# Optimization experiments

Measured on AMD Instinct MI355X. Metric: run time of the kernel, lower is better.

## Reference

```python
import jax, jax.numpy as jnp
import numpy as np

B, H, L, E = 32, 8, 512, 3
N_VARS = 8
TOP_P = 0.5
NOISE_EPS = 0.01
EPS = 1e-10


def setup_inputs() -> dict:
    key = jax.random.key(0)
    k1, k2, k3 = jax.random.split(key, 3)
    scale = 1.0 / np.sqrt(L)  # sane logits for softmax
    x = jax.random.normal(k1, (B, H, L, L), dtype=jnp.float32)
    gate_w = jax.random.normal(k2, (E, L), dtype=jnp.float32) * scale
    noise_w = jax.random.normal(k3, (E, L), dtype=jnp.float32) * scale
    return {"x": x, "gate_w": gate_w, "noise_w": noise_w}


def _build_masks(L, n_vars):
    # Vectorized version of the torch per-k loop building [L, 3, L] masks.
    N = L // n_vars
    j = jnp.arange(L)          # target position
    k = jnp.arange(L)[:, None]  # source position
    S = ((j % N == k % N) & (j != k)).astype(jnp.float32)   # same offset, different var
    T = ((j // N) == (k // N)).astype(jnp.float32)           # same variable block
    ST = 1.0 - S - T
    return jnp.stack([S, T, ST], axis=1)  # [L, 3, L]


def _noisy_top_p_gating(xf, gate_w, noise_w, key):
    # xf: [BH, L, L] -> logits [BH, L, E]
    clean_logits = jnp.einsum('ble,ne->bln', xf, gate_w)
    noise_stddev = jax.nn.softplus(jnp.einsum('ble,ne->bln', xf, noise_w)) + NOISE_EPS
    noisy_logits = clean_logits + jax.random.normal(key, clean_logits.shape, clean_logits.dtype) * noise_stddev
    probs = jax.nn.softmax(noisy_logits, axis=-1)  # softmax over experts (dim 2)
    # dynamic (entropy) loss: sum over L dim (dim=1), mean over rest
    loss_dynamic = -(probs * jnp.log(probs + EPS)).sum(axis=1).mean()
    # sort descending over experts
    order = jnp.argsort(-probs, axis=-1)
    sorted_probs = jnp.take_along_axis(probs, order, axis=-1)
    cum = jnp.cumsum(sorted_probs, axis=-1)
    mask = cum > TOP_P
    # keep the first expert that crosses the threshold
    thr_idx = jnp.argmax(mask.astype(jnp.int32), axis=-1)          # [BH, L]
    thr_mask = jnp.arange(E) == thr_idx[..., None]                 # one-hot bool
    mask = mask & ~thr_mask
    # scatter kept (mask==0) sorted positions back to original expert ids:
    # top_p_mask[..., sorted_indices[..., k]] = (mask[..., k] == 0)
    inv = jnp.argsort(order, axis=-1)
    top_p_mask = jnp.take_along_axis((~mask).astype(jnp.float32), inv, axis=-1)
    # importance loss on masked sorted probs summed over batch dim
    kept = jnp.where(mask, 0.0, sorted_probs)
    importance = kept.sum(axis=0)  # [L, E]
    loss_importance = jnp.var(importance, ddof=1) / (importance.mean() ** 2 + EPS)
    loss = loss_importance + 0.1 * loss_dynamic
    return top_p_mask, loss


def reference(x, gate_w, noise_w):
    Bx, Hx, Lx, _ = x.shape
    xf = x.reshape(Bx * Hx, Lx, Lx)
    gates, loss = _noisy_top_p_gating(xf, gate_w, noise_w, jax.random.key(42))
    gates = gates.reshape(Bx, Hx, Lx, E).astype(jnp.float32)
    masks = _build_masks(Lx, N_VARS)            # [L, 3, L]
    mask_base = jnp.eye(Lx, dtype=jnp.float32)[None, None]
    out = jnp.einsum('bhli,lid->bhld', gates, masks) + mask_base
    return (out, loss)
```

## Files before the change

kernel.cpp:

```cpp
#include <hip/hip_runtime.h>
#include <cstdint>
#include <cstddef>


namespace {

constexpr int kBH = 256;
constexpr int kL = 512;
constexpr int kE = 3;
constexpr int kRows = kBH * kL;
constexpr int kPad = 36;

typedef float v4f __attribute__((ext_vector_type(4)));

__device__ __forceinline__ uint32_t rotl32(uint32_t v, int n) {
  return (v << n) | (v >> (32 - n));
}

__device__ __forceinline__ void threefry2x32_k42(uint32_t& x0, uint32_t& x1) {
  const uint32_t ks0 = 0u;
  const uint32_t ks1 = 42u;
  const uint32_t ks2 = 0u ^ 42u ^ 0x1BD11BDAu;
  x0 += ks0; x1 += ks1;
#define TF_ROUND(r) { x0 += x1; x1 = rotl32(x1, (r)); x1 ^= x0; }
  TF_ROUND(13) TF_ROUND(15) TF_ROUND(26) TF_ROUND(6)
  x0 += ks1; x1 += ks2 + 1u;
  TF_ROUND(17) TF_ROUND(29) TF_ROUND(16) TF_ROUND(24)
  x0 += ks2; x1 += ks0 + 2u;
  TF_ROUND(13) TF_ROUND(15) TF_ROUND(26) TF_ROUND(6)
  x0 += ks0; x1 += ks1 + 3u;
  TF_ROUND(17) TF_ROUND(29) TF_ROUND(16) TF_ROUND(24)
  x0 += ks1; x1 += ks2 + 4u;
  TF_ROUND(13) TF_ROUND(15) TF_ROUND(26) TF_ROUND(6)
  x0 += ks2; x1 += ks0 + 5u;
#undef TF_ROUND
}

__device__ __forceinline__ uint32_t jax_random_bits(uint32_t flat_idx) {
  uint32_t x0 = 0u;
  uint32_t x1 = flat_idx;
  threefry2x32_k42(x0, x1);
  return x0 ^ x1;
}

__device__ float bits_to_normal(uint32_t bits) {
#pragma clang fp contract(off)
  const uint32_t fb = (bits >> 9) | 0x3F800000u;
  const float f = __uint_as_float(fb) - 1.0f;
  const float lo = -0.99999994f;
  float u = f * 2.0f + lo;
  u = fmaxf(lo, u);
  float w = -log1pf(-(u * u));
  float p;
  if (w < 5.0f) {
    w = w - 2.5f;
    p = 2.81022636e-08f;
    p = 3.43273939e-07f + p * w;
    p = -3.5233877e-06f + p * w;
    p = -4.39150654e-06f + p * w;
    p = 0.00021858087f + p * w;
    p = -0.00125372503f + p * w;
    p = -0.00417768164f + p * w;
    p = 0.246640727f + p * w;
    p = 1.50140941f + p * w;
  } else {
    w = sqrtf(w) - 3.0f;
    p = -0.000200214257f;
    p = 0.000100950558f + p * w;
    p = 0.00134934322f + p * w;
    p = -0.00367342844f + p * w;
    p = 0.00573950773f + p * w;
    p = -0.0076224613f + p * w;
    p = 0.00943887047f + p * w;
    p = 1.00167406f + p * w;
    p = 2.83297682f + p * w;
  }
  const float einv = p * u;
  return 1.41421354f * einv;
}

__device__ __forceinline__ float softplus_f32(float v) {
#pragma clang fp contract(off)
  const float amax = fmaxf(v, 0.0f);
  return amax + log1pf(expf(-fabsf(v)));
}

#define COMP16(BUF, KB)                                                     \
  {                                                                         \
    _Pragma("unroll")                                                       \
    for (int j_ = 0; j_ < 4; ++j_) {                                        \
      const int k_ = (KB) + j_ * 4;                                         \
      const float4 wg0 = *reinterpret_cast<const float4*>(gw + k_);         \
      const float4 wg1 = *reinterpret_cast<const float4*>(gw + kL + k_);    \
      const float4 wg2 = *reinterpret_cast<const float4*>(gw + 2*kL + k_);  \
      const float4 wn0 = *reinterpret_cast<const float4*>(nw + k_);         \
      const float4 wn1 = *reinterpret_cast<const float4*>(nw + kL + k_);    \
      const float4 wn2 = *reinterpret_cast<const float4*>(nw + 2*kL + k_);  \
      const float4 xq = BUF[j_];                                            \
      accg[0] = fmaf(xq.x, wg0.x, accg[0]);                                 \
      accg[1] = fmaf(xq.x, wg1.x, accg[1]);                                 \
      accg[2] = fmaf(xq.x, wg2.x, accg[2]);                                 \
      accn[0] = fmaf(xq.x, wn0.x, accn[0]);                                 \
      accn[1] = fmaf(xq.x, wn1.x, accn[1]);                                 \
      accn[2] = fmaf(xq.x, wn2.x, accn[2]);                                 \
      accg[0] = fmaf(xq.y, wg0.y, accg[0]);                                 \
      accg[1] = fmaf(xq.y, wg1.y, accg[1]);                                 \
      accg[2] = fmaf(xq.y, wg2.y, accg[2]);                                 \
      accn[0] = fmaf(xq.y, wn0.y, accn[0]);                                 \
      accn[1] = fmaf(xq.y, wn1.y, accn[1]);                                 \
      accn[2] = fmaf(xq.y, wn2.y, accn[2]);                                 \
      accg[0] = fmaf(xq.z, wg0.z, accg[0]);                                 \
      accg[1] = fmaf(xq.z, wg1.z, accg[1]);                                 \
      accg[2] = fmaf(xq.z, wg2.z, accg[2]);                                 \
      accn[0] = fmaf(xq.z, wn0.z, accn[0]);                                 \
      accn[1] = fmaf(xq.z, wn1.z, accn[1]);                                 \
      accn[2] = fmaf(xq.z, wn2.z, accn[2]);                                 \
      accg[0] = fmaf(xq.w, wg0.w, accg[0]);                                 \
      accg[1] = fmaf(xq.w, wg1.w, accg[1]);                                 \
      accg[2] = fmaf(xq.w, wg2.w, accg[2]);                                 \
      accn[0] = fmaf(xq.w, wn0.w, accn[0]);                                 \
      accn[1] = fmaf(xq.w, wn1.w, accn[1]);                                 \
      accn[2] = fmaf(xq.w, wn2.w, accn[2]);                                 \
    }                                                                       \
  }

#define STAGE_LOAD(ST, K0)                                                  \
  _Pragma("unroll")                                                         \
  for (int i_ = 0; i_ < 8; ++i_) {                                          \
    const int fi_ = i_ * 256 + t;                                           \
    const int row_ = fi_ >> 3;                                              \
    const int c4_ = fi_ & 7;                                                \
    ST[i_] = *reinterpret_cast<const float4*>(                              \
        xblk + (size_t)row_ * kL + (K0) + c4_ * 4);                         \
  }

#define STAGE_WRITE(ST, BUF)                                                \
  _Pragma("unroll")                                                         \
  for (int i_ = 0; i_ < 8; ++i_) {                                          \
    const int fi_ = i_ * 256 + t;                                           \
    const int row_ = fi_ >> 3;                                              \
    const int c4_ = fi_ & 7;                                                \
    *reinterpret_cast<float4*>(&s_x[BUF][row_ * kPad + c4_ * 4]) = ST[i_];  \
  }

__global__ __launch_bounds__(256) void gating_kernel(
    const float* __restrict__ x, const float* __restrict__ gw,
    const float* __restrict__ nw, float* __restrict__ g_out,
    float* __restrict__ kept_out, float* __restrict__ ent_out) {
  __shared__ float s_x[2][256 * kPad];
  const int t = threadIdx.x;
  const int r = blockIdx.x * 256 + t;
  const float* xblk = x + (size_t)blockIdx.x * 256 * kL;

  {
    float4 st[8];
    STAGE_LOAD(st, 0)
    STAGE_WRITE(st, 0)
  }
  __syncthreads();

  float accg[3] = {0.f, 0.f, 0.f};
  float accn[3] = {0.f, 0.f, 0.f};
  for (int tile = 0; tile < 16; ++tile) {
    const int k0 = tile * 32;
    float4 st[8];
    if (tile < 15) { STAGE_LOAD(st, k0 + 32) }
    {
#pragma clang fp contract(off)
      const float* xrow = &s_x[tile & 1][t * kPad];
      float4 bufL[4];
      bufL[0] = *reinterpret_cast<const float4*>(xrow);
      bufL[1] = *reinterpret_cast<const float4*>(xrow + 4);
      bufL[2] = *reinterpret_cast<const float4*>(xrow + 8);
      bufL[3] = *reinterpret_cast<const float4*>(xrow + 12);
      COMP16(bufL, k0)
      bufL[0] = *reinterpret_cast<const float4*>(xrow + 16);
      bufL[1] = *reinterpret_cast<const float4*>(xrow + 20);
      bufL[2] = *reinterpret_cast<const float4*>(xrow + 24);
      bufL[3] = *reinterpret_cast<const float4*>(xrow + 28);
      COMP16(bufL, k0 + 16)
    }
    if (tile < 15) { STAGE_WRITE(st, (tile + 1) & 1) }
    __syncthreads();
  }

  {
#pragma clang fp contract(off)
    float noisy[3];
    const uint32_t nbase = (uint32_t)r * 3u;
#pragma unroll
    for (int e = 0; e < 3; ++e) {
      const float cl = accg[e];
      const float sp = softplus_f32(accn[e]) + 0.01f;
      const float nz = bits_to_normal(jax_random_bits(nbase + (uint32_t)e));
      const float prod = nz * sp;
      noisy[e] = cl + prod;
    }
    const float m = fmaxf(noisy[0], fmaxf(noisy[1], noisy[2]));
    float uu[3];
    uu[0] = expf(noisy[0] - m);
    uu[1] = expf(noisy[1] - m);
    uu[2] = expf(noisy[2] - m);
    const float ssum = (uu[0] + uu[1]) + uu[2];
    float p[3];
    p[0] = uu[0] / ssum;
    p[1] = uu[1] / ssum;
    p[2] = uu[2] / ssum;

    int o0 = 0;
    if (p[1] > p[o0]) o0 = 1;
    if (p[2] > p[o0]) o0 = 2;
    const int i = (o0 == 0) ? 1 : 0;
    const int j = (o0 == 2) ? 1 : 2;
    const int o1 = (p[j] > p[i]) ? j : i;

    const float s0 = p[o0];
    const float s1 = p[o1];
    const bool keep2 = !(s0 > 0.5f);

    float g[3] = {0.f, 0.f, 0.f};
    g[o0] = 1.f;
    if (keep2) g[o1] = 1.f;

    float ent = 0.f;
    ent += p[0] * logf(p[0] + 1e-10f);
    ent += p[1] * logf(p[1] + 1e-10f);
    ent += p[2] * logf(p[2] + 1e-10f);

    const int bh = r >> 9;
    const int l = r & (kL - 1);
    g_out[r * 3 + 0] = g[0];
    g_out[r * 3 + 1] = g[1];
    g_out[r * 3 + 2] = g[2];
    kept_out[(0 * kL + l) * kBH + bh] = s0;
    kept_out[(1 * kL + l) * kBH + bh] = keep2 ? s1 : 0.f;
    kept_out[(2 * kL + l) * kBH + bh] = 0.f;
    ent_out[r] = -ent;
  }
}

__global__ __launch_bounds__(256) void loss_partial_kernel(
    const float* __restrict__ kept, const float* __restrict__ ent,
    double* __restrict__ imp_ws, double* __restrict__ ent_ws) {
  __shared__ double red[256];
  const int t = threadIdx.x;
  const int ln = t & 63;
  const int wg = blockIdx.x * 4 + (t >> 6);

#pragma unroll
  for (int rep = 0; rep < 3; ++rep) {
    const int q = wg + rep * 512;
    const float4 v = reinterpret_cast<const float4*>(kept + (size_t)q * kBH)[ln];
    double s = ((double)v.x + (double)v.y) + ((double)v.z + (double)v.w);
#pragma unroll
    for (int off = 32; off > 0; off >>= 1) s += __shfl_xor(s, off, 64);
    if (ln == 0) imp_ws[q] = s;
  }

  double a = 0.0;
#pragma unroll
  for (int it = 0; it < 4; ++it) {
    a += (double)ent[blockIdx.x * 1024 + it * 256 + t];
  }
  red[t] = a;
  __syncthreads();
  for (int off = 128; off > 0; off >>= 1) {
    if (t < off) red[t] += red[t + off];
    __syncthreads();
  }
  if (t == 0) ent_ws[blockIdx.x] = red[0];
}

__global__ __launch_bounds__(256) void out_kernel(
    const float* __restrict__ g, const double* __restrict__ imp_ws,
    const double* __restrict__ ent_ws, float* __restrict__ out,
    float* __restrict__ loss_out) {
  const int td = threadIdx.x;

  if (blockIdx.x == 0) {
    __shared__ double red[256];
    __shared__ double s_mean;
    double a = 0.0;
    for (int i = td; i < kL * kE; i += 256) a += imp_ws[i];
    red[td] = a;
    __syncthreads();
    for (int off = 128; off > 0; off >>= 1) {
      if (td < off) red[td] += red[td + off];
      __syncthreads();
    }
    if (td == 0) s_mean = red[0] / (double)(kL * kE);
    __syncthreads();
    const double mean = s_mean;

    double sq = 0.0;
    for (int i = td; i < kL * kE; i += 256) {
      const double d = imp_ws[i] - mean;
      sq += d * d;
    }
    red[td] = sq;
    __syncthreads();
    for (int off = 128; off > 0; off >>= 1) {
      if (td < off) red[td] += red[td + off];
      __syncthreads();
    }
    const double var_sum = red[0];
    __syncthreads();

    double e = 0.0;
    for (int i = td; i < 128; i += 256) e += ent_ws[i];
    red[td] = e;
    __syncthreads();
    for (int off = 128; off > 0; off >>= 1) {
      if (td < off) red[td] += red[td + off];
      __syncthreads();
    }
    if (td == 0) {
      const double var = var_sum / (double)(kL * kE - 1);
      const double loss_imp = var / (mean * mean + 1e-10);
      const double loss_dyn = red[0] / 768.0;
      loss_out[0] = (float)(loss_imp + 0.1 * loss_dyn);
    }
  }

  const int r = blockIdx.x * 8 + (td >> 5);
  const int l = r & (kL - 1);
  const float g0 = g[r * 3 + 0];
  const float g1 = g[r * 3 + 1];
  const float g2 = g[r * 3 + 2];
  const int lblk = l >> 6;
  const int loff = l & 63;
  float* orow = out + (size_t)r * kL;
  const int c0 = (td & 31) * 4;
#pragma unroll
  for (int j = 0; j < 4; ++j) {
    const int d0 = c0 + j * 128;
    v4f vals;
#pragma unroll
    for (int k = 0; k < 4; ++k) {
      const int d = d0 + k;
      float v;
      if (((d & 63) == loff) && (d != l)) v = g0;
      else if ((d >> 6) == lblk) v = g1;
      else v = g2;
      if (d == l) v += 1.0f;
      vals[k] = v;
    }
    __builtin_nontemporal_store(vals, reinterpret_cast<v4f*>(orow + d0));
  }
}

}

extern "C" void kernel_launch(void* const* d_in, const int* in_sizes, int n_in,
                              void* d_out, int out_size, void* d_ws, size_t ws_size,
                              hipStream_t stream) {
  (void)in_sizes; (void)n_in; (void)out_size; (void)ws_size;
  const float* x = (const float*)d_in[0];
  const float* gw = (const float*)d_in[1];
  const float* nw = (const float*)d_in[2];
  float* out = (float*)d_out;

  float* ws = (float*)d_ws;
  float* ws_g = ws;
  float* ws_kept = ws + (size_t)kRows * 3;
  float* ws_ent = ws + (size_t)kRows * 6;
  double* ws_imp = (double*)(ws + (size_t)kRows * 7);
  double* ws_entp = ws_imp + kL * kE;

  gating_kernel<<<kRows / 256, 256, 0, stream>>>(x, gw, nw, ws_g, ws_kept, ws_ent);
  loss_partial_kernel<<<128, 256, 0, stream>>>(ws_kept, ws_ent, ws_imp, ws_entp);
  out_kernel<<<kRows / 8, 256, 0, stream>>>(ws_g, ws_imp, ws_entp, out,
                                            out + (size_t)kBH * kL * kL);
}
```

Baseline: 114.8 us.

## Fuse loss partial reductions into gating kernel via double atomics

Removes the separate loss_partial kernel. The gating kernel now atomically accumulates per-position importance sums in double precision, and each block reduces its entropy in shared memory before one atomic add to a global total. A memset zeroes the accumulators before launch. This saves a launch and the round trip of the kept and entropy arrays through global memory, at the cost of contended atomics (256 adds per address) and non-deterministic summation order.

```diff
diff --git a/kernel.cpp b/kernel.cpp
--- a/kernel.cpp
+++ b/kernel.cpp
@@ -146,8 +146,9 @@
 __global__ __launch_bounds__(256) void gating_kernel(
     const float* __restrict__ x, const float* __restrict__ gw,
     const float* __restrict__ nw, float* __restrict__ g_out,
-    float* __restrict__ kept_out, float* __restrict__ ent_out) {
+    double* __restrict__ imp_ws, double* __restrict__ ent_total) {
   __shared__ float s_x[2][256 * kPad];
+  __shared__ double s_red[256];
   const int t = threadIdx.x;
   const int r = blockIdx.x * 256 + t;
   const float* xblk = x + (size_t)blockIdx.x * 256 * kL;
@@ -184,6 +185,7 @@
     __syncthreads();
   }
 
+  float ent_f;
   {
 #pragma clang fp contract(off)
     float noisy[3];
@@ -226,54 +228,28 @@
     ent += p[0] * logf(p[0] + 1e-10f);
     ent += p[1] * logf(p[1] + 1e-10f);
     ent += p[2] * logf(p[2] + 1e-10f);
-
-    const int bh = r >> 9;
+    ent_f = -ent;
+
     const int l = r & (kL - 1);
     g_out[r * 3 + 0] = g[0];
     g_out[r * 3 + 1] = g[1];
     g_out[r * 3 + 2] = g[2];
-    kept_out[(0 * kL + l) * kBH + bh] = s0;
-    kept_out[(1 * kL + l) * kBH + bh] = keep2 ? s1 : 0.f;
-    kept_out[(2 * kL + l) * kBH + bh] = 0.f;
-    ent_out[r] = -ent;
-  }
-}
-
-__global__ __launch_bounds__(256) void loss_partial_kernel(
-    const float* __restrict__ kept, const float* __restrict__ ent,
-    double* __restrict__ imp_ws, double* __restrict__ ent_ws) {
-  __shared__ double red[256];
-  const int t = threadIdx.x;
-  const int ln = t & 63;
-  const int wg = blockIdx.x * 4 + (t >> 6);
-
-#pragma unroll
-  for (int rep = 0; rep < 3; ++rep) {
-    const int q = wg + rep * 512;
-    const float4 v = reinterpret_cast<const float4*>(kept + (size_t)q * kBH)[ln];
-    double s = ((double)v.x + (double)v.y) + ((double)v.z + (double)v.w);
-#pragma unroll
-    for (int off = 32; off > 0; off >>= 1) s += __shfl_xor(s, off, 64);
-    if (ln == 0) imp_ws[q] = s;
-  }
-
-  double a = 0.0;
-#pragma unroll
-  for (int it = 0; it < 4; ++it) {
-    a += (double)ent[blockIdx.x * 1024 + it * 256 + t];
-  }
-  red[t] = a;
+    atomicAdd(&imp_ws[0 * kL + l], (double)s0);
+    if (keep2) atomicAdd(&imp_ws[1 * kL + l], (double)s1);
+  }
+
+  s_red[t] = (double)ent_f;
   __syncthreads();
   for (int off = 128; off > 0; off >>= 1) {
-    if (t < off) red[t] += red[t + off];
-    __syncthreads();
-  }
-  if (t == 0) ent_ws[blockIdx.x] = red[0];
+    if (t < off) s_red[t] += s_red[t + off];
+    __syncthreads();
+  }
+  if (t == 0) atomicAdd(ent_total, s_red[0]);
 }
 
 __global__ __launch_bounds__(256) void out_kernel(
     const float* __restrict__ g, const double* __restrict__ imp_ws,
-    const double* __restrict__ ent_ws, float* __restrict__ out,
+    const double* __restrict__ ent_total, float* __restrict__ out,
     float* __restrict__ loss_out) {
   const int td = threadIdx.x;
 
@@ -303,21 +279,10 @@
       if (td < off) red[td] += red[td + off];
       __syncthreads();
     }
-    const double var_sum = red[0];
-    __syncthreads();
-
-    double e = 0.0;
-    for (int i = td; i < 128; i += 256) e += ent_ws[i];
-    red[td] = e;
-    __syncthreads();
-    for (int off = 128; off > 0; off >>= 1) {
-      if (td < off) red[td] += red[td + off];
-      __syncthreads();
-    }
     if (td == 0) {
-      const double var = var_sum / (double)(kL * kE - 1);
+      const double var = red[0] / (double)(kL * kE - 1);
       const double loss_imp = var / (mean * mean + 1e-10);
-      const double loss_dyn = red[0] / 768.0;
+      const double loss_dyn = ent_total[0] / 768.0;
       loss_out[0] = (float)(loss_imp + 0.1 * loss_dyn);
     }
   }
@@ -362,13 +327,13 @@
 
   float* ws = (float*)d_ws;
   float* ws_g = ws;
-  float* ws_kept = ws + (size_t)kRows * 3;
-  float* ws_ent = ws + (size_t)kRows * 6;
-  double* ws_imp = (double*)(ws + (size_t)kRows * 7);
-  double* ws_entp = ws_imp + kL * kE;
-
-  gating_kernel<<<kRows / 256, 256, 0, stream>>>(x, gw, nw, ws_g, ws_kept, ws_ent);
-  loss_partial_kernel<<<128, 256, 0, stream>>>(ws_kept, ws_ent, ws_imp, ws_entp);
-  out_kernel<<<kRows / 8, 256, 0, stream>>>(ws_g, ws_imp, ws_entp, out,
+  double* ws_imp = (double*)(ws + (size_t)kRows * 3);
+  double* ws_enttot = ws_imp + kL * kE;
+
+  hipMemsetAsync(ws_imp, 0, (kL * kE + 1) * sizeof(double), stream);
+
+  gating_kernel<<<kRows / 256, 256, 0, stream>>>(x, gw, nw, ws_g, ws_imp,
+                                                 ws_enttot);
+  out_kernel<<<kRows / 8, 256, 0, stream>>>(ws_g, ws_imp, ws_enttot, out,
                                             out + (size_t)kBH * kL * kL);
 }
```

After: 118.7 us. +3.4%, slower.
